# Performance work log

Hardware: AMD Instinct MI355X
Metric: run time of the kernel (lower is better)

## Reference

```python
import jax, jax.numpy as jnp
import numpy as np

NC = 19
CH16, CH32 = 1024, 2048
B, H, W = 4, 64, 64
EPS = 1e-5


def bn_relu(x, gamma, beta):
    # Train-mode BatchNorm (batch statistics, as in torch default) + ReLU.
    axes = (0,) + tuple(range(2, x.ndim))  # reduce over batch + spatial
    mean = jnp.mean(x, axes, keepdims=True)
    var = jnp.var(x, axes, keepdims=True)
    shp = (1, -1) + (1,) * (x.ndim - 2)
    return jax.nn.relu((x - mean) * jax.lax.rsqrt(var + EPS) * gamma.reshape(shp) + beta.reshape(shp))


def setup_inputs() -> dict:
    key = jax.random.key(0)
    ks = jax.random.split(key, 10)
    def p(k, shape, fan):
        return jax.random.normal(k, shape, jnp.float32) / np.float32(np.sqrt(fan))
    ones = lambda c: jnp.ones((c,), jnp.float32)
    zeros = lambda c: jnp.zeros((c,), jnp.float32)
    return {
        "x": jax.random.normal(ks[0], (B, CH32, H, W), jnp.float32),
        "low_level_feature": jax.random.normal(ks[1], (B, CH16, H, W), jnp.float32),
        "W_L": p(ks[2], (NC, CH16), CH16), "b_L": zeros(NC),
        "W_X": p(ks[3], (512, CH32, 3, 3), CH32 * 9), "g_X": ones(512), "be_X": zeros(512),
        "W_phi": p(ks[4], (256, 512), 512), "g_phi": ones(256), "be_phi": zeros(256),
        "W_psi": p(ks[5], (256, 512), 512), "g_psi": ones(256), "be_psi": zeros(256),
        "W_delta": p(ks[6], (256, 512), 512), "g_delta": ones(256), "be_delta": zeros(256),
        "W_rho": p(ks[7], (512, 256), 256), "g_rho": ones(512), "be_rho": zeros(512),
        "W_g": p(ks[8], (512, 1024), 1024), "g_g": ones(512), "be_g": zeros(512),
        "W_out": p(ks[9], (NC, 512), 512), "b_out": zeros(NC),
    }


def reference(x, low_level_feature, W_L, b_L, W_X, g_X, be_X,
              W_phi, g_phi, be_phi, W_psi, g_psi, be_psi,
              W_delta, g_delta, be_delta, W_rho, g_rho, be_rho,
              W_g, g_g, be_g, W_out, b_out):
    b, _, h, w = x.shape
    # X = conv2d(2048->512, 3x3) + BN + ReLU
    Xf = jax.lax.conv_general_dilated(x, W_X, (1, 1), 'SAME',
                                      dimension_numbers=('NCHW', 'OIHW', 'NCHW'))
    Xf = bn_relu(Xf, g_X, be_X)                          # [b,512,h,w]
    # L = 1x1 conv (with bias) -> soft object regions
    L = jnp.einsum('bchw,nc->bnhw', low_level_feature, W_L) + b_L[None, :, None, None]
    l_flat = L.reshape(b, L.shape[1], -1)                # [b,nc,N]
    M = jax.nn.softmax(l_flat, axis=-1)                  # softmax over N
    X_flat = Xf.reshape(b, 512, -1)                      # [b,512,N]
    # f_k = (M @ X_flat^T)^T : object region features [b,512,nc]
    f_k = jnp.einsum('bkn,bcn->bck', M, X_flat)
    # phi/psi/delta: 1x1 conv1d + BN + ReLU
    query = bn_relu(jnp.einsum('oc,bck->bok', W_phi, f_k), g_phi, be_phi)      # [b,256,nc]
    key_ = bn_relu(jnp.einsum('oc,bcn->bon', W_psi, X_flat), g_psi, be_psi)    # [b,256,N]
    logit = jnp.einsum('bqk,bqn->bkn', query, key_)      # [b,nc,N]
    attn = jax.nn.softmax(logit, axis=1)                 # softmax over nc (dim 1)
    delta = bn_relu(jnp.einsum('oc,bck->bok', W_delta, f_k), g_delta, be_delta)  # [b,256,nc]
    attn_sum = jnp.einsum('bqk,bkn->bqn', delta, attn)   # [b,256,N]
    X_obj = bn_relu(jnp.einsum('oq,bqn->bon', W_rho, attn_sum), g_rho, be_rho)
    X_obj = X_obj.reshape(b, 512, h, w)
    concat = jnp.concatenate([Xf, X_obj], axis=1)        # [b,1024,h,w]
    X_bar = bn_relu(jnp.einsum('oc,bchw->bohw', W_g, concat), g_g, be_g)
    out = jnp.einsum('nc,bchw->bnhw', W_out, X_bar) + b_out[None, :, None, None]
    return out
```

## Files before the change

### kernel.cpp

```cpp
#include <hip/hip_runtime.h>
#include <hip/hip_bf16.h>
#include <cstdint>
#include <cstddef>

#define EPSV 1e-5f

typedef float f32x4 __attribute__((ext_vector_type(4)));
typedef _Float16 f16x8 __attribute__((ext_vector_type(8)));
typedef unsigned short ushortx8 __attribute__((ext_vector_type(8)));

__device__ __forceinline__ unsigned short f2h(float f) {
  _Float16 h = (_Float16)f;
  return *reinterpret_cast<unsigned short*>(&h);
}

__device__ __forceinline__ void gload16(const void* g, void* l) {
  __builtin_amdgcn_global_load_lds(
      (const __attribute__((address_space(1))) void*)g,
      (__attribute__((address_space(3))) void*)l, 16, 0, 0);
}

__global__ __launch_bounds__(256) void ocr_halo_zero(unsigned short* __restrict__ xT) {
  int e = blockIdx.x, b = blockIdx.y, t = threadIdx.x;
  ushortx8 z = {0, 0, 0, 0, 0, 0, 0, 0};
  if (e < 2) {
    int row = e ? 65 : 0;
    ushortx8* p = (ushortx8*)(xT + (size_t)(b * 66 + row) * 66 * 2048);
    for (int i = t; i < 66 * 256; i += 256) p[i] = z;
  } else {
    int col = (e == 3) ? 65 : 0;
    for (int idx = t; idx < 64 * 256; idx += 256) {
      int r = (idx >> 8) + 1, v = idx & 255;
      ((ushortx8*)(xT + ((size_t)(b * 66 + r) * 66 + col) * 2048))[v] = z;
    }
  }
}

__global__ __launch_bounds__(256) void ocr_cvt_x(const float* __restrict__ x,
                                                 unsigned short* __restrict__ xT) {
  __shared__ float tile[64][65];
  int icb = blockIdx.x, h = blockIdx.y, b = blockIdx.z, t = threadIdx.x;
  const float* xp = x + ((size_t)b * 2048 + icb * 64) * 4096 + h * 64;
  #pragma unroll
  for (int r = 0; r < 16; ++r) {
    int icl = r * 4 + (t >> 6), w = t & 63;
    tile[icl][w] = xp[(size_t)icl * 4096 + w];
  }
  __syncthreads();
  #pragma unroll
  for (int it = 0; it < 2; ++it) {
    int w = it * 32 + (t >> 3), cb = (t & 7) * 8;
    ushortx8 o;
    #pragma unroll
    for (int j = 0; j < 8; ++j) o[j] = f2h(tile[cb + j][w]);
    *(ushortx8*)&xT[(((size_t)b * 66 + h + 1) * 66 + (w + 1)) * 2048 + icb * 64 + cb] = o;
  }
}

__global__ __launch_bounds__(256) void ocr_cvt_w(const float* __restrict__ Wx,
                                                 unsigned short* __restrict__ WT) {
  int oc = blockIdx.x >> 3;
  int ic = (blockIdx.x & 7) * 256 + threadIdx.x;
  const float* wp = Wx + ((size_t)oc * 2048 + ic) * 9;
  float v[9];
  #pragma unroll
  for (int t = 0; t < 9; ++t) v[t] = wp[t];
  #pragma unroll
  for (int t = 0; t < 9; ++t)
    WT[((size_t)t * 512 + oc) * 2048 + ic] = f2h(v[t]);
}

__global__ __launch_bounds__(256) void ocr_cvt_h2(const float* __restrict__ inA,
                                                  unsigned short* __restrict__ outA,
                                                  const float* __restrict__ inB,
                                                  unsigned short* __restrict__ outB) {
  int i = blockIdx.x * 256 + threadIdx.x;
  if (i < 131072) outA[i] = f2h(inA[i]);
  if (i < 524288) outB[i] = f2h(inB[i]);
}

__global__ __launch_bounds__(1024, 4) void ocr_conv_mfma(const unsigned short* __restrict__ xT,
                                                         const unsigned short* __restrict__ WT,
                                                         float* __restrict__ Xf) {
  __shared__ __align__(16) char lds_raw[163840];
  float* red = (float*)lds_raw;

  const int t = threadIdx.x;
  const int wv = t >> 6, lane = t & 63;
  const int kg = lane >> 4, lc = lane & 15;
  const int ws = wv & 7, kh = wv >> 3;

  const int hg  = blockIdx.x & 7;
  const int b   = (blockIdx.x >> 3) & 3;
  const int oct = blockIdx.x >> 5;
  const int oc0 = oct * 64, h0 = hg * 8;

  const char* gp[5]; int lo[5];
  #pragma unroll
  for (int i = 0; i < 5; ++i) {
    int c = wv * 5 + i;
    lo[i] = c * 1024;
    if (c < 38) {
      int cell = c * 64 + lane; if (cell > 2375) cell = 2375;
      int r = cell / 66, col = cell - r * 66; if (col > 63) col = 63;
      int tap = r >> 2, kgs = r & 3;
      gp[i] = (const char*)WT + (size_t)(((tap * 512 + oc0 + col) * 2048) + kgs * 8) * 2;
    } else {
      int c2 = c - 38;
      int cell = c2 * 64 + lane; if (cell > 2639) cell = 2639;
      int r = cell / 66, col = cell - r * 66;
      int row = r >> 2, kgs = r & 3;
      gp[i] = (const char*)xT + (size_t)((((b * 66 + h0 + row) * 66 + col) * 2048) + kgs * 8) * 2;
    }
  }

  f32x4 acc[4][4] = {};

  #pragma unroll
  for (int i = 0; i < 5; ++i) gload16(gp[i], lds_raw + lo[i]);
  __syncthreads();

  int cur = 0;
  #pragma unroll 1
  for (int step = 0; step < 64; ++step) {
    if (step < 63) {
      unsigned adv = (unsigned)(step + 1) * 64u;
      int nxt = (cur ^ 1) * 81920;
      #pragma unroll
      for (int i = 0; i < 5; ++i) gload16(gp[i] + adv, lds_raw + nxt + lo[i]);
    }
    const short* As = (const short*)(lds_raw + cur * 81920);
    const short* Bs = (const short*)(lds_raw + cur * 81920 + 38912);
    #pragma unroll
    for (int j = 0; j < 5; ++j) {
      const int tap = kh * 4 + j;
      const int dh = tap / 3, dw = tap - dh * 3;
      f16x8 av[4];
      #pragma unroll
      for (int mi = 0; mi < 4; ++mi)
        av[mi] = *(const f16x8*)&As[((tap * 4 + kg) * 66 + mi * 16 + lc) * 8];
      const int row = ws + dh;
      const int nw0 = (tap == 4) ? (kh ? 2 : 0) : 0;
      const int nwN = (tap == 4) ? (nw0 + 2) : 4;
      #pragma unroll
      for (int nw = 0; nw < 4; ++nw) {
        if (nw >= nw0 && nw < nwN) {
          f16x8 bv = *(const f16x8*)&Bs[((row * 4 + kg) * 66 + nw * 16 + lc + dw) * 8];
          #pragma unroll
          for (int mi = 0; mi < 4; ++mi)
            acc[mi][nw] = __builtin_amdgcn_mfma_f32_16x16x32_f16(av[mi], bv, acc[mi][nw], 0, 0, 0);
        }
      }
    }
    __syncthreads();
    cur ^= 1;
  }

  if (kh == 1) {
    #pragma unroll
    for (int mi = 0; mi < 4; ++mi)
      #pragma unroll
      for (int nw = 0; nw < 4; ++nw)
        *(f32x4*)&red[(((ws * 16 + mi * 4 + nw) * 64) + lane) * 4] = acc[mi][nw];
  }
  __syncthreads();
  if (kh == 0) {
    const int h = h0 + ws;
    #pragma unroll
    for (int mi = 0; mi < 4; ++mi) {
      #pragma unroll
      for (int nw = 0; nw < 4; ++nw) {
        f32x4 other = *(const f32x4*)&red[(((ws * 16 + mi * 4 + nw) * 64) + lane) * 4];
        f32x4 s = acc[mi][nw] + other;
        #pragma unroll
        for (int r = 0; r < 4; ++r) {
          int oc = oc0 + mi * 16 + (lane >> 4) * 4 + r;
          int w = nw * 16 + lc;
          Xf[(((size_t)b * 512 + oc) * 64 + h) * 64 + w] = s[r];
        }
      }
    }
  }
}

template<int K, int OT, int NT, int NWM, int NWN, int LDB>
__global__ __launch_bounds__(256) void ocr_gemm_h(const unsigned short* __restrict__ Ah,
                                                  const unsigned short* __restrict__ Bh,
                                                  float* __restrict__ Cm, int O) {
  static_assert(NT == 128, "NT fixed");
  constexpr int MI = OT / NWM / 16;
  constexpr int NI = NT / NWN / 16;
  constexpr int SA = OT + 2, SB = NT + 2;
  constexpr int ACELL = 4 * OT / 256;
  constexpr int ABUF = 4 * SA * 8;
  constexpr int BBUF = 4 * SB * 8;
  constexpr int NS = K / 32;
  constexpr int LPW = ACELL + 2;
  __shared__ __align__(16) short As_s[2 * ABUF];
  __shared__ __align__(16) short Bs_s[2 * BBUF];

  const int t = threadIdx.x;
  const int wv = t >> 6, lane = t & 63;
  const int kg = lane >> 4, lc = lane & 15;
  const int wm = wv / NWN, wn = wv % NWN;

  const int n0 = blockIdx.x * NT, o0 = blockIdx.y * OT, b = blockIdx.z;

  const char* aBase[ACELL]; int aLds[ACELL];
  #pragma unroll
  for (int r = 0; r < ACELL; ++r) {
    int flat0 = r * 256 + (t & 448);
    int flat  = flat0 + lane;
    int kgs = flat / OT, ol = flat % OT;
    aBase[r] = (const char*)(Ah + ((size_t)(o0 + ol)) * K + kgs * 8);
    aLds[r] = ((flat0 / OT) * SA + (flat0 % OT)) * 16;
  }
  const char* bBase[2]; int bLds[2];
  #pragma unroll
  for (int r = 0; r < 2; ++r) {
    int flat0 = r * 256 + (t & 448);
    int flat  = flat0 + lane;
    int kgs = flat >> 7, nl = flat & 127;
    bBase[r] = (const char*)(Bh + ((size_t)b * 4096 + n0 + nl) * LDB + kgs * 8);
    bLds[r] = ((flat0 >> 7) * SB + (flat0 & 127)) * 16;
  }

  f32x4 acc[MI][NI] = {};
  #pragma unroll
  for (int r = 0; r < ACELL; ++r) gload16(aBase[r], (char*)As_s + aLds[r]);
  #pragma unroll
  for (int r = 0; r < 2; ++r) gload16(bBase[r], (char*)Bs_s + bLds[r]);
  asm volatile("s_waitcnt vmcnt(0)" ::: "memory");
  __builtin_amdgcn_s_barrier();

  int cur = 0;
  #pragma unroll 1
  for (int step = 0; step < NS; ++step) {
    if (step + 1 < NS) {
      unsigned adv = (unsigned)(step + 1) * 64u;
      int nA = (cur ^ 1) * ABUF * 2, nB = (cur ^ 1) * BBUF * 2;
      #pragma unroll
      for (int r = 0; r < ACELL; ++r) gload16(aBase[r] + adv, (char*)As_s + nA + aLds[r]);
      #pragma unroll
      for (int r = 0; r < 2; ++r) gload16(bBase[r] + adv, (char*)Bs_s + nB + bLds[r]);
      if constexpr (LPW == 3) asm volatile("s_waitcnt vmcnt(3)" ::: "memory");
      else                    asm volatile("s_waitcnt vmcnt(4)" ::: "memory");
    } else {
      asm volatile("s_waitcnt vmcnt(0)" ::: "memory");
    }
    __builtin_amdgcn_s_barrier();

    const short* As = As_s + cur * ABUF;
    const short* Bsc = Bs_s + cur * BBUF;
    f16x8 av[MI], bv[NI];
    #pragma unroll
    for (int mi = 0; mi < MI; ++mi)
      av[mi] = *(const f16x8*)&As[(kg * SA + wm * (MI * 16) + mi * 16 + lc) * 8];
    #pragma unroll
    for (int ni = 0; ni < NI; ++ni)
      bv[ni] = *(const f16x8*)&Bsc[(kg * SB + wn * (NI * 16) + ni * 16 + lc) * 8];
    __builtin_amdgcn_s_setprio(1);
    #pragma unroll
    for (int mi = 0; mi < MI; ++mi)
      #pragma unroll
      for (int ni = 0; ni < NI; ++ni)
        acc[mi][ni] = __builtin_amdgcn_mfma_f32_16x16x32_f16(av[mi], bv[ni], acc[mi][ni], 0, 0, 0);
    __builtin_amdgcn_s_setprio(0);
    asm volatile("s_waitcnt lgkmcnt(0)" ::: "memory");
    __builtin_amdgcn_sched_barrier(0);
    __builtin_amdgcn_s_barrier();
    cur ^= 1;
  }
  #pragma unroll
  for (int mi = 0; mi < MI; ++mi) {
    #pragma unroll
    for (int ni = 0; ni < NI; ++ni) {
      int n = n0 + wn * (NI * 16) + ni * 16 + lc;
      #pragma unroll
      for (int r = 0; r < 4; ++r) {
        int oc = o0 + wm * (MI * 16) + mi * 16 + (lane >> 4) * 4 + r;
        Cm[((size_t)b * O + oc) * 4096 + n] = acc[mi][ni][r];
      }
    }
  }
}

__global__ __launch_bounds__(256) void ocr_t2h(const float* __restrict__ in,
                                               const float* __restrict__ scale,
                                               const float* __restrict__ shift,
                                               unsigned short* __restrict__ out,
                                               int C, int coff) {
  __shared__ float tile[64][65];
  int n0 = blockIdx.x * 64, c0 = blockIdx.y * 64, b = blockIdx.z;
  int t = threadIdx.x;
  #pragma unroll
  for (int r = 0; r < 16; ++r) {
    int c_l = r * 4 + (t >> 6), n_l = t & 63;
    tile[c_l][n_l] = in[((size_t)(b * C + c0 + c_l)) * 4096 + n0 + n_l];
  }
  __syncthreads();
  int n_l = t >> 2, cb = (t & 3) * 16;
  ushortx8 o0v, o1v;
  #pragma unroll
  for (int j = 0; j < 8; ++j) {
    int c = c0 + cb + j;
    o0v[j] = f2h(fmaxf(0.f, tile[cb + j][n_l] * scale[c] + shift[c]));
  }
  #pragma unroll
  for (int j = 0; j < 8; ++j) {
    int c = c0 + cb + 8 + j;
    o1v[j] = f2h(fmaxf(0.f, tile[cb + 8 + j][n_l] * scale[c] + shift[c]));
  }
  size_t base = ((size_t)b * 4096 + n0 + n_l) * 1024 + coff + c0 + cb;
  *(ushortx8*)&out[base] = o0v;
  *(ushortx8*)&out[base + 8] = o1v;
}

__global__ __launch_bounds__(256) void ocr_chan_stats(const float* __restrict__ buf,
                                                      const float* __restrict__ gamma,
                                                      const float* __restrict__ beta,
                                                      float* __restrict__ scale,
                                                      float* __restrict__ shift, int C) {
  int c = blockIdx.x, t = threadIdx.x;
  float s = 0.f, q = 0.f;
  for (int b = 0; b < 4; ++b) {
    const float* p = buf + ((size_t)b * C + c) * 4096;
    for (int i = t; i < 4096; i += 256) { float v = p[i]; s += v; q += v * v; }
  }
  __shared__ float ls[256], lq[256];
  ls[t] = s; lq[t] = q; __syncthreads();
  for (int off = 128; off > 0; off >>= 1) {
    if (t < off) { ls[t] += ls[t + off]; lq[t] += lq[t + off]; }
    __syncthreads();
  }
  if (t == 0) {
    float mean = ls[0] / 16384.f;
    float var  = lq[0] / 16384.f - mean * mean;
    float sc   = gamma[c] * rsqrtf(var + EPSV);
    scale[c] = sc; shift[c] = beta[c] - mean * sc;
  }
}

__global__ __launch_bounds__(256) void ocr_lproj(const float* __restrict__ llf,
                                                 const float* __restrict__ WL,
                                                 const float* __restrict__ bL,
                                                 float* __restrict__ L) {
  int h = blockIdx.x, b = blockIdx.y;
  int t = threadIdx.x, w = t & 63, csub = t >> 6;
  float acc[19];
  #pragma unroll
  for (int k = 0; k < 19; ++k) acc[k] = 0.f;
  const float* base = llf + ((size_t)b * 1024 + csub * 256) * 4096 + h * 64 + w;
  #pragma unroll 1
  for (int c4 = 0; c4 < 64; ++c4) {
    float lv[4];
    #pragma unroll
    for (int i = 0; i < 4; ++i) lv[i] = base[(size_t)(c4 + i * 64) * 4096];
    #pragma unroll
    for (int i = 0; i < 4; ++i) {
      const float* wl = &WL[csub * 256 + c4 + i * 64];
      #pragma unroll
      for (int k = 0; k < 19; ++k) acc[k] += wl[k * 1024] * lv[i];
    }
  }
  __shared__ float red[4][64][19];
  #pragma unroll
  for (int k = 0; k < 19; ++k) red[csub][w][k] = acc[k];
  __syncthreads();
  if (csub == 0) {
    #pragma unroll
    for (int k = 0; k < 19; ++k) {
      float s = red[0][w][k] + red[1][w][k] + red[2][w][k] + red[3][w][k] + bL[k];
      L[((size_t)b * 19 + k) * 4096 + h * 64 + w] = s;
    }
  }
}

__global__ __launch_bounds__(256) void ocr_softmax4096(float* __restrict__ buf) {
  int row = blockIdx.x, t = threadIdx.x;
  float* p = buf + (size_t)row * 4096;
  __shared__ float ls[256];
  float m = -1e30f;
  for (int i = t; i < 4096; i += 256) m = fmaxf(m, p[i]);
  ls[t] = m; __syncthreads();
  for (int off = 128; off > 0; off >>= 1) { if (t < off) ls[t] = fmaxf(ls[t], ls[t + off]); __syncthreads(); }
  m = ls[0]; __syncthreads();
  float s = 0.f;
  for (int i = t; i < 4096; i += 256) { float e = __expf(p[i] - m); p[i] = e; s += e; }
  ls[t] = s; __syncthreads();
  for (int off = 128; off > 0; off >>= 1) { if (t < off) ls[t] += ls[t + off]; __syncthreads(); }
  float inv = 1.f / ls[0];
  for (int i = t; i < 4096; i += 256) p[i] *= inv;
}

__global__ __launch_bounds__(256) void ocr_fk(const float* __restrict__ M,
                                              const float* __restrict__ Xf,
                                              const float* __restrict__ scale,
                                              const float* __restrict__ shift,
                                              float* __restrict__ fk) {
  int c = blockIdx.x, b = blockIdx.y, t = threadIdx.x;
  float acc[19];
  #pragma unroll
  for (int k = 0; k < 19; ++k) acc[k] = 0.f;
  const float* xp = Xf + ((size_t)b * 512 + c) * 4096;
  const float* mp = M + (size_t)b * 19 * 4096;
  float sc = scale[c], sh = shift[c];
  for (int n = t; n < 4096; n += 256) {
    float xv = fmaxf(0.f, xp[n] * sc + sh);
    #pragma unroll
    for (int k = 0; k < 19; ++k) acc[k] += mp[k * 4096 + n] * xv;
  }
  __shared__ float red[19 * 256];
  #pragma unroll
  for (int k = 0; k < 19; ++k) red[k * 256 + t] = acc[k];
  __syncthreads();
  for (int off = 128; off > 0; off >>= 1) {
    if (t < off) {
      #pragma unroll
      for (int k = 0; k < 19; ++k) red[k * 256 + t] += red[k * 256 + t + off];
    }
    __syncthreads();
  }
  if (t < 19) fk[((size_t)b * 512 + c) * 19 + t] = red[t * 256];
}

__global__ __launch_bounds__(256) void ocr_qd2(const float* __restrict__ Wphi,
                                               const float* __restrict__ Wdelta,
                                               const float* __restrict__ fk,
                                               float* __restrict__ qry,
                                               float* __restrict__ dlt) {
  int blk = blockIdx.x;
  const float* Wm = (blk < 76) ? Wphi : Wdelta;
  float* out = (blk < 76) ? qry : dlt;
  int tid = (blk < 76 ? blk : blk - 76) * 256 + threadIdx.x;
  if (tid >= 4 * 256 * 19) return;
  int k = tid % 19, o = (tid / 19) % 256, b = tid / (19 * 256);
  const float* fp = fk + (size_t)b * 512 * 19 + k;
  const float* wp = Wm + (size_t)o * 512;
  float acc = 0.f;
  for (int c = 0; c < 512; ++c) acc += wp[c] * fp[c * 19];
  out[tid] = acc;
}

__global__ __launch_bounds__(128) void ocr_bn76x2(float* __restrict__ qry,
                                                  float* __restrict__ dlt,
                                                  const float* __restrict__ g_phi,
                                                  const float* __restrict__ be_phi,
                                                  const float* __restrict__ g_delta,
                                                  const float* __restrict__ be_delta) {
  bool second = blockIdx.x >= 256;
  int o = blockIdx.x & 255, t = threadIdx.x;
  float* buf = second ? dlt : qry;
  const float* gamma = second ? g_delta : g_phi;
  const float* beta  = second ? be_delta : be_phi;
  bool act = t < 76;
  float v = 0.f;
  size_t idx = 0;
  if (act) {
    int b = t / 19, k = t % 19;
    idx = ((size_t)b * 256 + o) * 19 + k;
    v = buf[idx];
  }
  __shared__ float ls[128], lq[128];
  ls[t] = act ? v : 0.f; lq[t] = act ? v * v : 0.f; __syncthreads();
  for (int off = 64; off > 0; off >>= 1) { if (t < off) { ls[t] += ls[t + off]; lq[t] += lq[t + off]; } __syncthreads(); }
  __shared__ float s_sc, s_sh;
  if (t == 0) {
    float mean = ls[0] / 76.f;
    float var  = lq[0] / 76.f - mean * mean;
    float sc   = gamma[o] * rsqrtf(var + EPSV);
    s_sc = sc; s_sh = beta[o] - mean * sc;
  }
  __syncthreads();
  if (act) buf[idx] = fmaxf(0.f, v * s_sc + s_sh);
}

__global__ __launch_bounds__(256) void ocr_attn(const float* __restrict__ query,
                                                const float* __restrict__ key,
                                                const float* __restrict__ scale,
                                                const float* __restrict__ shift,
                                                float* __restrict__ attn) {
  int n0 = blockIdx.x * 64, b = blockIdx.y;
  int t = threadIdx.x, nl = t & 63, qsub = t >> 6;
  __shared__ float ql[256 * 19];
  for (int i = t; i < 256 * 19; i += 256) ql[i] = query[(size_t)b * 256 * 19 + i];
  __syncthreads();
  float acc[19];
  #pragma unroll
  for (int k = 0; k < 19; ++k) acc[k] = 0.f;
  const float* kp = key + ((size_t)b * 256 + qsub * 64) * 4096 + n0 + nl;
  #pragma unroll 1
  for (int q4 = 0; q4 < 64; q4 += 4) {
    float kv[4];
    #pragma unroll
    for (int i = 0; i < 4; ++i) kv[i] = kp[(size_t)(q4 + i) * 4096];
    #pragma unroll
    for (int i = 0; i < 4; ++i) {
      int ch = qsub * 64 + q4 + i;
      float kva = fmaxf(0.f, kv[i] * scale[ch] + shift[ch]);
      const float* qq = &ql[ch * 19];
      #pragma unroll
      for (int k = 0; k < 19; ++k) acc[k] += qq[k] * kva;
    }
  }
  __shared__ float red[4][64][19];
  #pragma unroll
  for (int k = 0; k < 19; ++k) red[qsub][nl][k] = acc[k];
  __syncthreads();
  if (qsub == 0) {
    float v[19]; float m = -1e30f;
    #pragma unroll
    for (int k = 0; k < 19; ++k) {
      v[k] = red[0][nl][k] + red[1][nl][k] + red[2][nl][k] + red[3][nl][k];
      m = fmaxf(m, v[k]);
    }
    float s = 0.f;
    #pragma unroll
    for (int k = 0; k < 19; ++k) { v[k] = __expf(v[k] - m); s += v[k]; }
    float inv = 1.f / s;
    #pragma unroll
    for (int k = 0; k < 19; ++k)
      attn[((size_t)b * 19 + k) * 4096 + n0 + nl] = v[k] * inv;
  }
}

__global__ __launch_bounds__(256) void ocr_wd(const float* __restrict__ Wrho,
                                              const float* __restrict__ dlt,
                                              float* __restrict__ Wd) {
  int tid = blockIdx.x * 256 + threadIdx.x;
  if (tid >= 4 * 512 * 19) return;
  int k = tid % 19, o = (tid / 19) % 512, b = tid / (19 * 512);
  const float* dp = dlt + (size_t)b * 256 * 19 + k;
  const float* wp = Wrho + (size_t)o * 256;
  float acc = 0.f;
  for (int q = 0; q < 256; ++q) acc += wp[q] * dp[q * 19];
  Wd[tid] = acc;
}

__global__ __launch_bounds__(384) void ocr_gram(const float* __restrict__ attn,
                                                float* __restrict__ G,
                                                float* __restrict__ RS) {
  __shared__ float al[19][513];
  int n0 = blockIdx.x * 512, b = blockIdx.y, t = threadIdx.x;
  for (int i = t; i < 19 * 512; i += 384) {
    int k = i >> 9, n = i & 511;
    al[k][n] = attn[((size_t)b * 19 + k) * 4096 + n0 + n];
  }
  __syncthreads();
  if (t < 361) {
    int k1 = t / 19, k2 = t % 19;
    float s = 0.f;
    for (int n = 0; n < 512; ++n) s += al[k1][n] * al[k2][n];
    atomicAdd(&G[(b * 19 + k1) * 19 + k2], s);
  } else if (t < 380) {
    int k = t - 361;
    float s = 0.f;
    for (int n = 0; n < 512; ++n) s += al[k][n];
    atomicAdd(&RS[b * 19 + k], s);
  }
}

__global__ __launch_bounds__(512) void ocr_xobj_fin(const float* __restrict__ Wd,
                                                    const float* __restrict__ G,
                                                    const float* __restrict__ RS,
                                                    const float* __restrict__ gamma,
                                                    const float* __restrict__ beta,
                                                    float* __restrict__ scale,
                                                    float* __restrict__ shift) {
  int o = threadIdx.x;
  float s = 0.f, q = 0.f;
  for (int b = 0; b < 4; ++b) {
    float wd[19];
    #pragma unroll
    for (int k = 0; k < 19; ++k) wd[k] = Wd[((size_t)b * 512 + o) * 19 + k];
    const float* g = &G[b * 361];
    const float* rs = &RS[b * 19];
    #pragma unroll
    for (int k = 0; k < 19; ++k) s += wd[k] * rs[k];
    for (int k1 = 0; k1 < 19; ++k1) {
      float tacc = 0.f;
      #pragma unroll
      for (int k2 = 0; k2 < 19; ++k2) tacc += g[k1 * 19 + k2] * wd[k2];
      q += wd[k1] * tacc;
    }
  }
  float mean = s / 16384.f;
  float var  = q / 16384.f - mean * mean;
  float sc   = gamma[o] * rsqrtf(var + EPSV);
  scale[o] = sc; shift[o] = beta[o] - mean * sc;
}

__global__ __launch_bounds__(512) void ocr_xobj_apply(const float* __restrict__ Wd,
                                                      const float* __restrict__ attn,
                                                      const float* __restrict__ scale,
                                                      const float* __restrict__ shift,
                                                      unsigned short* __restrict__ ch) {
  __shared__ float al[19][256];
  int n0 = blockIdx.x * 256, b = blockIdx.y, o = threadIdx.x;
  for (int idx = o; idx < 19 * 256; idx += 512) {
    int k = idx >> 8, nl = idx & 255;
    al[k][nl] = attn[((size_t)b * 19 + k) * 4096 + n0 + nl];
  }
  float wd[19];
  #pragma unroll
  for (int k = 0; k < 19; ++k) wd[k] = Wd[((size_t)b * 512 + o) * 19 + k];
  float sc = scale[o], sh = shift[o];
  __syncthreads();
  #pragma unroll 1
  for (int nl = 0; nl < 256; ++nl) {
    float v = 0.f;
    #pragma unroll
    for (int k = 0; k < 19; ++k) v += wd[k] * al[k][nl];
    v = fmaxf(0.f, v * sc + sh);
    ch[((size_t)b * 4096 + n0 + nl) * 1024 + 512 + o] = f2h(v);
  }
}

__global__ __launch_bounds__(256) void ocr_out(const float* __restrict__ Wout,
                                               const float* __restrict__ bout,
                                               const float* __restrict__ Xbar,
                                               const float* __restrict__ scale,
                                               const float* __restrict__ shift,
                                               float* __restrict__ out) {
  int n0 = blockIdx.x * 64, b = blockIdx.y;
  int t = threadIdx.x, nl = t & 63, csub = t >> 6;
  float acc[19];
  #pragma unroll
  for (int k = 0; k < 19; ++k) acc[k] = 0.f;
  const float* base = Xbar + ((size_t)b * 512 + csub * 128) * 4096 + n0 + nl;
  #pragma unroll 1
  for (int c4 = 0; c4 < 128; c4 += 4) {
    float xv[4];
    #pragma unroll
    for (int i = 0; i < 4; ++i) xv[i] = base[(size_t)(c4 + i) * 4096];
    #pragma unroll
    for (int i = 0; i < 4; ++i) {
      int chn = csub * 128 + c4 + i;
      float a = fmaxf(0.f, xv[i] * scale[chn] + shift[chn]);
      #pragma unroll
      for (int k = 0; k < 19; ++k) acc[k] += Wout[k * 512 + chn] * a;
    }
  }
  __shared__ float red[4][64][19];
  #pragma unroll
  for (int k = 0; k < 19; ++k) red[csub][nl][k] = acc[k];
  __syncthreads();
  if (csub == 0) {
    #pragma unroll
    for (int k = 0; k < 19; ++k) {
      float s = red[0][nl][k] + red[1][nl][k] + red[2][nl][k] + red[3][nl][k] + bout[k];
      out[((size_t)b * 19 + k) * 4096 + n0 + nl] = s;
    }
  }
}

extern "C" void kernel_launch(void* const* d_in, const int* in_sizes, int n_in,
                              void* d_out, int out_size, void* d_ws, size_t ws_size,
                              hipStream_t stream) {
  const float* x    = (const float*)d_in[0];
  const float* llf  = (const float*)d_in[1];
  const float* W_L  = (const float*)d_in[2];
  const float* b_L  = (const float*)d_in[3];
  const float* W_X  = (const float*)d_in[4];
  const float* g_X  = (const float*)d_in[5];
  const float* be_X = (const float*)d_in[6];
  const float* W_phi = (const float*)d_in[7];
  const float* g_phi = (const float*)d_in[8];
  const float* be_phi = (const float*)d_in[9];
  const float* W_psi = (const float*)d_in[10];
  const float* g_psi = (const float*)d_in[11];
  const float* be_psi = (const float*)d_in[12];
  const float* W_delta = (const float*)d_in[13];
  const float* g_delta = (const float*)d_in[14];
  const float* be_delta = (const float*)d_in[15];
  const float* W_rho = (const float*)d_in[16];
  const float* g_rho = (const float*)d_in[17];
  const float* be_rho = (const float*)d_in[18];
  const float* W_g  = (const float*)d_in[19];
  const float* g_g  = (const float*)d_in[20];
  const float* be_g = (const float*)d_in[21];
  const float* W_out = (const float*)d_in[22];
  const float* b_out = (const float*)d_in[23];

  float* ws = (float*)d_ws;
  float* Xf = ws;
  float* U  = ws + 8388608;
  unsigned short* xT = (unsigned short*)U;
  unsigned short* WT = (unsigned short*)(U + 17842176);
  unsigned short* concat_h = (unsigned short*)U;
  float* key  = U + 8388608;
  float* Xbar = U + 12582912;
  float* SM   = U + 22560768;
  float* M     = SM;
  float* attnb = SM + 311296;
  float* fk    = SM + 622592;
  float* qry   = SM + 661504;
  float* dlt   = SM + 680960;
  float* Wd    = SM + 700416;
  float* st    = SM + 739328;
  unsigned short* Wpsi_h = (unsigned short*)(SM + 743424);
  unsigned short* Wg_h   = (unsigned short*)(SM + 808960);
  float* Gm    = SM + 1071104;
  float* RSm   = SM + 1072548;
  float* scX = st,        *shX = st + 512;
  float* scP = st + 1024, *shP = st + 1280;
  float* scR = st + 1536, *shR = st + 2048;
  float* scG = st + 2560, *shG = st + 3072;

  ocr_halo_zero<<<dim3(4, 4), 256, 0, stream>>>(xT);
  ocr_cvt_x<<<dim3(32, 64, 4), 256, 0, stream>>>(x, xT);
  ocr_cvt_w<<<dim3(4096), 256, 0, stream>>>(W_X, WT);
  ocr_cvt_h2<<<dim3(2048), 256, 0, stream>>>(W_psi, Wpsi_h, W_g, Wg_h);
  hipMemsetAsync(Gm, 0, 1520 * sizeof(float), stream);

  ocr_conv_mfma<<<dim3(256), 1024, 0, stream>>>(xT, WT, Xf);

  ocr_chan_stats<<<dim3(512), 256, 0, stream>>>(Xf, g_X, be_X, scX, shX, 512);
  ocr_t2h<<<dim3(64, 8, 4), 256, 0, stream>>>(Xf, scX, shX, concat_h, 512, 0);
  ocr_lproj<<<dim3(64, 4), 256, 0, stream>>>(llf, W_L, b_L, M);
  ocr_softmax4096<<<dim3(76), 256, 0, stream>>>(M);
  ocr_fk<<<dim3(512, 4), 256, 0, stream>>>(M, Xf, scX, shX, fk);
  ocr_qd2<<<dim3(152), 256, 0, stream>>>(W_phi, W_delta, fk, qry, dlt);
  ocr_bn76x2<<<dim3(512), 128, 0, stream>>>(qry, dlt, g_phi, be_phi, g_delta, be_delta);
  ocr_gemm_h<512, 64, 128, 2, 2, 1024><<<dim3(32, 4, 4), 256, 0, stream>>>(Wpsi_h, concat_h, key, 256);
  ocr_chan_stats<<<dim3(256), 256, 0, stream>>>(key, g_psi, be_psi, scP, shP, 256);
  ocr_attn<<<dim3(64, 4), 256, 0, stream>>>(qry, key, scP, shP, attnb);
  ocr_wd<<<dim3(152), 256, 0, stream>>>(W_rho, dlt, Wd);
  ocr_gram<<<dim3(8, 4), 384, 0, stream>>>(attnb, Gm, RSm);
  ocr_xobj_fin<<<dim3(1), 512, 0, stream>>>(Wd, Gm, RSm, g_rho, be_rho, scR, shR);
  ocr_xobj_apply<<<dim3(16, 4), 512, 0, stream>>>(Wd, attnb, scR, shR, concat_h);
  ocr_gemm_h<1024, 128, 128, 2, 2, 1024><<<dim3(32, 4, 4), 256, 0, stream>>>(Wg_h, concat_h, Xbar, 512);
  ocr_chan_stats<<<dim3(512), 256, 0, stream>>>(Xbar, g_g, be_g, scG, shG, 512);
  ocr_out<<<dim3(64, 4), 256, 0, stream>>>(W_out, b_out, Xbar, scG, shG, (float*)d_out);
}
```

Before: 737.4 us.

## Fuse BN channel statistics into conv and GEMM epilogues via atomics

Result: no change. 747.9 us (+1.4%).

```diff
diff --git a/kernel.cpp b/kernel.cpp
--- a/kernel.cpp
+++ b/kernel.cpp
@@ -79,9 +79,25 @@
   if (i < 524288) outB[i] = f2h(inB[i]);
 }
 
+__global__ __launch_bounds__(256) void ocr_finstats(const float* __restrict__ sum,
+                                                    const float* __restrict__ sq,
+                                                    const float* __restrict__ gamma,
+                                                    const float* __restrict__ beta,
+                                                    float* __restrict__ scale,
+                                                    float* __restrict__ shift, int C) {
+  int c = blockIdx.x * 256 + threadIdx.x;
+  if (c >= C) return;
+  float mean = sum[c] * (1.f / 16384.f);
+  float var  = sq[c] * (1.f / 16384.f) - mean * mean;
+  float sc   = gamma[c] * rsqrtf(var + EPSV);
+  scale[c] = sc; shift[c] = beta[c] - mean * sc;
+}
+
 __global__ __launch_bounds__(1024, 4) void ocr_conv_mfma(const unsigned short* __restrict__ xT,
                                                          const unsigned short* __restrict__ WT,
-                                                         float* __restrict__ Xf) {
+                                                         float* __restrict__ Xf,
+                                                         float* __restrict__ sumX,
+                                                         float* __restrict__ sqX) {
   __shared__ __align__(16) char lds_raw[163840];
   float* red = (float*)lds_raw;
 
@@ -101,14 +117,14 @@
     int c = wv * 5 + i;
     lo[i] = c * 1024;
     if (c < 38) {
-      int cell = c * 64 + lane; if (cell > 2375) cell = 2375;
-      int r = cell / 66, col = cell - r * 66; if (col > 63) col = 63;
+      int cell = c * 64 + lane; if (cell > 2411) cell = 2411;
+      int r = cell / 67, col = cell - r * 67; if (col > 63) col = 63;
       int tap = r >> 2, kgs = r & 3;
       gp[i] = (const char*)WT + (size_t)(((tap * 512 + oc0 + col) * 2048) + kgs * 8) * 2;
     } else {
       int c2 = c - 38;
-      int cell = c2 * 64 + lane; if (cell > 2639) cell = 2639;
-      int r = cell / 66, col = cell - r * 66;
+      int cell = c2 * 64 + lane; if (cell > 2679) cell = 2679;
+      int r = cell / 67, col = cell - r * 67; if (col > 65) col = 65;
       int row = r >> 2, kgs = r & 3;
       gp[i] = (const char*)xT + (size_t)((((b * 66 + h0 + row) * 66 + col) * 2048) + kgs * 8) * 2;
     }
@@ -138,14 +154,14 @@
       f16x8 av[4];
       #pragma unroll
       for (int mi = 0; mi < 4; ++mi)
-        av[mi] = *(const f16x8*)&As[((tap * 4 + kg) * 66 + mi * 16 + lc) * 8];
+        av[mi] = *(const f16x8*)&As[((tap * 4 + kg) * 67 + mi * 16 + lc) * 8];
       const int row = ws + dh;
       const int nw0 = (tap == 4) ? (kh ? 2 : 0) : 0;
       const int nwN = (tap == 4) ? (nw0 + 2) : 4;
       #pragma unroll
       for (int nw = 0; nw < 4; ++nw) {
         if (nw >= nw0 && nw < nwN) {
-          f16x8 bv = *(const f16x8*)&Bs[((row * 4 + kg) * 66 + nw * 16 + lc + dw) * 8];
+          f16x8 bv = *(const f16x8*)&Bs[((row * 4 + kg) * 67 + nw * 16 + lc + dw) * 8];
           #pragma unroll
           for (int mi = 0; mi < 4; ++mi)
             acc[mi][nw] = __builtin_amdgcn_mfma_f32_16x16x32_f16(av[mi], bv, acc[mi][nw], 0, 0, 0);
@@ -166,6 +182,7 @@
   __syncthreads();
   if (kh == 0) {
     const int h = h0 + ws;
+    float ps[4][4] = {}, pq[4][4] = {};
     #pragma unroll
     for (int mi = 0; mi < 4; ++mi) {
       #pragma unroll
@@ -177,6 +194,25 @@
           int oc = oc0 + mi * 16 + (lane >> 4) * 4 + r;
           int w = nw * 16 + lc;
           Xf[(((size_t)b * 512 + oc) * 64 + h) * 64 + w] = s[r];
+          ps[mi][r] += s[r];
+          pq[mi][r] += s[r] * s[r];
+        }
+      }
+    }
+    #pragma unroll
+    for (int mi = 0; mi < 4; ++mi) {
+      #pragma unroll
+      for (int r = 0; r < 4; ++r) {
+        float a = ps[mi][r], q = pq[mi][r];
+        #pragma unroll
+        for (int m = 1; m <= 8; m <<= 1) {
+          a += __shfl_xor(a, m);
+          q += __shfl_xor(q, m);
+        }
+        if (lc == 0) {
+          int oc = oc0 + mi * 16 + (lane >> 4) * 4 + r;
+          atomicAdd(&sumX[oc], a);
+          atomicAdd(&sqX[oc], q);
         }
       }
     }
@@ -186,7 +222,9 @@
 template<int K, int OT, int NT, int NWM, int NWN, int LDB>
 __global__ __launch_bounds__(256) void ocr_gemm_h(const unsigned short* __restrict__ Ah,
                                                   const unsigned short* __restrict__ Bh,
-                                                  float* __restrict__ Cm, int O) {
+                                                  float* __restrict__ Cm, int O,
+                                                  float* __restrict__ Sm,
+                                                  float* __restrict__ Sq) {
   static_assert(NT == 128, "NT fixed");
   constexpr int MI = OT / NWM / 16;
   constexpr int NI = NT / NWN / 16;
@@ -283,6 +321,28 @@
       }
     }
   }
+  #pragma unroll
+  for (int mi = 0; mi < MI; ++mi) {
+    #pragma unroll
+    for (int r = 0; r < 4; ++r) {
+      float a = 0.f, q = 0.f;
+      #pragma unroll
+      for (int ni = 0; ni < NI; ++ni) {
+        float v = acc[mi][ni][r];
+        a += v; q += v * v;
+      }
+      #pragma unroll
+      for (int m = 1; m <= 8; m <<= 1) {
+        a += __shfl_xor(a, m);
+        q += __shfl_xor(q, m);
+      }
+      if (lc == 0) {
+        int oc = o0 + wm * (MI * 16) + mi * 16 + (lane >> 4) * 4 + r;
+        atomicAdd(&Sm[oc], a);
+        atomicAdd(&Sq[oc], q);
+      }
+    }
+  }
 }
 
 __global__ __launch_bounds__(256) void ocr_t2h(const float* __restrict__ in,
@@ -314,31 +374,6 @@
   size_t base = ((size_t)b * 4096 + n0 + n_l) * 1024 + coff + c0 + cb;
   *(ushortx8*)&out[base] = o0v;
   *(ushortx8*)&out[base + 8] = o1v;
-}
-
-__global__ __launch_bounds__(256) void ocr_chan_stats(const float* __restrict__ buf,
-                                                      const float* __restrict__ gamma,
-                                                      const float* __restrict__ beta,
-                                                      float* __restrict__ scale,
-                                                      float* __restrict__ shift, int C) {
-  int c = blockIdx.x, t = threadIdx.x;
-  float s = 0.f, q = 0.f;
-  for (int b = 0; b < 4; ++b) {
-    const float* p = buf + ((size_t)b * C + c) * 4096;
-    for (int i = t; i < 4096; i += 256) { float v = p[i]; s += v; q += v * v; }
-  }
-  __shared__ float ls[256], lq[256];
-  ls[t] = s; lq[t] = q; __syncthreads();
-  for (int off = 128; off > 0; off >>= 1) {
-    if (t < off) { ls[t] += ls[t + off]; lq[t] += lq[t + off]; }
-    __syncthreads();
-  }
-  if (t == 0) {
-    float mean = ls[0] / 16384.f;
-    float var  = lq[0] / 16384.f - mean * mean;
-    float sc   = gamma[c] * rsqrtf(var + EPSV);
-    scale[c] = sc; shift[c] = beta[c] - mean * sc;
-  }
 }
 
 __global__ __launch_bounds__(256) void ocr_lproj(const float* __restrict__ llf,
@@ -702,6 +737,12 @@
   unsigned short* Wg_h   = (unsigned short*)(SM + 808960);
   float* Gm    = SM + 1071104;
   float* RSm   = SM + 1072548;
+  float* sumX  = SM + 1072624;
+  float* sqX   = SM + 1073136;
+  float* sumP  = SM + 1073648;
+  float* sqP   = SM + 1073904;
+  float* sumG  = SM + 1074160;
+  float* sqG   = SM + 1074672;
   float* scX = st,        *shX = st + 512;
   float* scP = st + 1024, *shP = st + 1280;
   float* scR = st + 1536, *shR = st + 2048;
@@ -711,25 +752,25 @@
   ocr_cvt_x<<<dim3(32, 64, 4), 256, 0, stream>>>(x, xT);
   ocr_cvt_w<<<dim3(4096), 256, 0, stream>>>(W_X, WT);
   ocr_cvt_h2<<<dim3(2048), 256, 0, stream>>>(W_psi, Wpsi_h, W_g, Wg_h);
-  hipMemsetAsync(Gm, 0, 1520 * sizeof(float), stream);
-
-  ocr_conv_mfma<<<dim3(256), 1024, 0, stream>>>(xT, WT, Xf);
-
-  ocr_chan_stats<<<dim3(512), 256, 0, stream>>>(Xf, g_X, be_X, scX, shX, 512);
+  hipMemsetAsync(Gm, 0, 4080 * sizeof(float), stream);
+
+  ocr_conv_mfma<<<dim3(256), 1024, 0, stream>>>(xT, WT, Xf, sumX, sqX);
+
+  ocr_finstats<<<dim3(2), 256, 0, stream>>>(sumX, sqX, g_X, be_X, scX, shX, 512);
   ocr_t2h<<<dim3(64, 8, 4), 256, 0, stream>>>(Xf, scX, shX, concat_h, 512, 0);
   ocr_lproj<<<dim3(64, 4), 256, 0, stream>>>(llf, W_L, b_L, M);
   ocr_softmax4096<<<dim3(76), 256, 0, stream>>>(M);
   ocr_fk<<<dim3(512, 4), 256, 0, stream>>>(M, Xf, scX, shX, fk);
   ocr_qd2<<<dim3(152), 256, 0, stream>>>(W_phi, W_delta, fk, qry, dlt);
   ocr_bn76x2<<<dim3(512), 128, 0, stream>>>(qry, dlt, g_phi, be_phi, g_delta, be_delta);
-  ocr_gemm_h<512, 64, 128, 2, 2, 1024><<<dim3(32, 4, 4), 256, 0, stream>>>(Wpsi_h, concat_h, key, 256);
-  ocr_chan_stats<<<dim3(256), 256, 0, stream>>>(key, g_psi, be_psi, scP, shP, 256);
+  ocr_gemm_h<512, 64, 128, 2, 2, 1024><<<dim3(32, 4, 4), 256, 0, stream>>>(Wpsi_h, concat_h, key, 256, sumP, sqP);
+  ocr_finstats<<<dim3(1), 256, 0, stream>>>(sumP, sqP, g_psi, be_psi, scP, shP, 256);
   ocr_attn<<<dim3(64, 4), 256, 0, stream>>>(qry, key, scP, shP, attnb);
   ocr_wd<<<dim3(152), 256, 0, stream>>>(W_rho, dlt, Wd);
   ocr_gram<<<dim3(8, 4), 384, 0, stream>>>(attnb, Gm, RSm);
   ocr_xobj_fin<<<dim3(1), 512, 0, stream>>>(Wd, Gm, RSm, g_rho, be_rho, scR, shR);
   ocr_xobj_apply<<<dim3(16, 4), 512, 0, stream>>>(Wd, attnb, scR, shR, concat_h);
-  ocr_gemm_h<1024, 128, 128, 2, 2, 1024><<<dim3(32, 4, 4), 256, 0, stream>>>(Wg_h, concat_h, Xbar, 512);
-  ocr_chan_stats<<<dim3(512), 256, 0, stream>>>(Xbar, g_g, be_g, scG, shG, 512);
+  ocr_gemm_h<1024, 128, 128, 2, 2, 1024><<<dim3(32, 4, 4), 256, 0, stream>>>(Wg_h, concat_h, Xbar, 512, sumG, sqG);
+  ocr_finstats<<<dim3(2), 256, 0, stream>>>(sumG, sqG, g_g, be_g, scG, shG, 512);
   ocr_out<<<dim3(64, 4), 256, 0, stream>>>(W_out, b_out, Xbar, scG, shG, (float*)d_out);
 }
```
